# Optimization experiments

Hardware: AMD Instinct MI355X
Metric: run time of the kernel (lower is better)

## Reference

```python
import jax, jax.numpy as jnp
import numpy as np

B, N, DIM = 4, 2048, 512
H, DH = 8, 64  # n_heads, dim_head; inner = H*DH = 512
SCALE = DH ** -0.5


def setup_inputs() -> dict:
    key = jax.random.key(0)
    k1, k2, k3 = jax.random.split(key, 3)
    inner = H * DH
    X = jax.random.normal(k1, (B, N, DIM), dtype=jnp.float32)
    W_qkv = jax.random.normal(k2, (DIM, 3 * inner), dtype=jnp.float32) * (DIM ** -0.5)
    W_out = jax.random.normal(k3, (inner, DIM), dtype=jnp.float32) * (inner ** -0.5)
    b_out = jnp.zeros((DIM,), dtype=jnp.float32)
    return {"X": X, "W_qkv": W_qkv, "W_out": W_out, "b_out": b_out}


def reference(X, W_qkv, W_out, b_out):
    # X: (b, n, dim)
    qkv = X @ W_qkv                      # (b, n, 3*h*d)
    q, k, v = jnp.split(qkv, 3, axis=-1)
    def to_heads(t):
        b, n, _ = t.shape
        return t.reshape(b, n, H, DH).transpose(0, 2, 1, 3)  # (b, h, n, d)
    q, k, v = to_heads(q), to_heads(k), to_heads(v)
    # NOTE: original computes scores[n, m] = k_n . q_m and softmaxes over m (query axis)
    scores = jnp.einsum('bhnd,bhmd->bhnm', k, q) * SCALE     # (b, h, n_k, m_q)
    att = jax.nn.softmax(scores, axis=-1)
    # out token axis is the KEY index n: out[n, d] = sum_e att[n, e] * v[e, d]
    out = jnp.einsum('bhne,bhed->bhnd', att, v)              # (b, h, n, d)
    out = out.transpose(0, 2, 1, 3).reshape(X.shape[0], X.shape[1], H * DH)  # (b, n, h*d)
    return out @ W_out + b_out
```

## Files before the change

kernel.cpp:

```cpp
#include <hip/hip_runtime.h>
#include <hip/hip_bf16.h>

typedef __bf16 bf16_t;
typedef bf16_t bf16x8 __attribute__((ext_vector_type(8)));
typedef bf16_t bf16x4v __attribute__((ext_vector_type(4)));
typedef float f32x4 __attribute__((ext_vector_type(4)));
typedef float f32x16 __attribute__((ext_vector_type(16)));
typedef int i32x4 __attribute__((ext_vector_type(4)));

#define B_SZ 4
#define N_TOK 2048
#define DIM 512
#define H_N 8
#define DH 64
#define INNER 512
#define M_ROWS 8192
#define NQKV 1536
#define K_FOLD 0.18033688011112042f

#define GLD_LDS16(gp, lp)                                          \
  __builtin_amdgcn_global_load_lds(                                \
      (const __attribute__((address_space(1))) void*)(gp),         \
      (__attribute__((address_space(3))) void*)(lp), 16, 0, 0)

__device__ __forceinline__ float fexp2(float x) {
#if __has_builtin(__builtin_amdgcn_exp2f)
  return __builtin_amdgcn_exp2f(x);
#else
  float r;
  asm volatile("v_exp_f32 %0, %1\n\ts_nop 1" : "=v"(r) : "v"(x));
  return r;
#endif
}

__device__ __forceinline__ int cvtpk_bf16(float lo, float hi) {
  int r;
  asm("v_cvt_pk_bf16_f32 %0, %1, %2" : "=v"(r) : "v"(lo), "v"(hi));
  return r;
}

__device__ __forceinline__ void permswap32(int& a, int& b) {
  asm volatile("v_permlane32_swap_b32 %0, %1" : "+v"(a), "+v"(b));
}


__global__ void f32_to_bf16_kernel(const float* __restrict__ src,
                                   bf16_t* __restrict__ dst, int n4) {
  int i = blockIdx.x * blockDim.x + threadIdx.x;
  int stride = gridDim.x * blockDim.x;
  for (; i < n4; i += stride) {
    float4 f = reinterpret_cast<const float4*>(src)[i];
    bf16x4v o;
    o.x = (bf16_t)f.x; o.y = (bf16_t)f.y; o.z = (bf16_t)f.z; o.w = (bf16_t)f.w;
    reinterpret_cast<bf16x4v*>(dst)[i] = o;
  }
}

__global__ void transpose_f32_to_bf16_kernel(const float* __restrict__ src,
                                             bf16_t* __restrict__ dst, int R, int C) {
  int t = blockIdx.x * blockDim.x + threadIdx.x;
  if (t >= R * C) return;
  int r = t / C, c = t - r * C;
  dst[(size_t)c * R + r] = (bf16_t)src[t];
}

template <int MODE>
__global__ __launch_bounds__(256) void gemm_bf16_kernel(
    const bf16_t* __restrict__ A, const bf16_t* __restrict__ Bt,
    int M, int Nn, int K,
    bf16_t* __restrict__ qb, bf16_t* __restrict__ kb, bf16_t* __restrict__ vtb,
    float* __restrict__ outF, const float* __restrict__ bias) {
  __shared__ bf16_t As[128 * 64];
  __shared__ bf16_t Bs[128 * 64];

  const int tid = threadIdx.x;
  const int lane = tid & 63;
  const int wave = tid >> 6;
  const int g = lane >> 4, c = lane & 15;
  const int wm = (wave >> 1) * 64, wn = (wave & 1) * 64;
  const int m0 = blockIdx.x * 128, n0 = blockIdx.y * 128;

  f32x4 acc[4][4] = {};

  for (int k0 = 0; k0 < K; k0 += 64) {
    __syncthreads();
    #pragma unroll
    for (int i = 0; i < 4; ++i) {
      int blk = i * 256 + tid;
      int row = blk >> 3;
      int cb = (blk & 7) ^ (row & 7);
      int base = (i * 256 + wave * 64) * 8;
      GLD_LDS16(A + (size_t)(m0 + row) * K + k0 + cb * 8, &As[base]);
      GLD_LDS16(Bt + (size_t)(n0 + row) * K + k0 + cb * 8, &Bs[base]);
    }
    __syncthreads();
    __builtin_amdgcn_s_setprio(1);
    #pragma unroll
    for (int ks = 0; ks < 2; ++ks) {
      bf16x8 af[4], bfr[4];
      #pragma unroll
      for (int i = 0; i < 4; ++i) {
        af[i] = *reinterpret_cast<const bf16x8*>(
            &As[(wm + i * 16 + c) * 64 + (((ks * 4 + g) ^ (c & 7)) * 8)]);
        bfr[i] = *reinterpret_cast<const bf16x8*>(
            &Bs[(wn + i * 16 + c) * 64 + (((ks * 4 + g) ^ (c & 7)) * 8)]);
      }
      #pragma unroll
      for (int mi = 0; mi < 4; ++mi)
        #pragma unroll
        for (int ni = 0; ni < 4; ++ni)
          acc[mi][ni] = __builtin_amdgcn_mfma_f32_16x16x32_bf16(
              af[mi], bfr[ni], acc[mi][ni], 0, 0, 0);
    }
    __builtin_amdgcn_s_setprio(0);
  }

  #pragma unroll
  for (int mi = 0; mi < 4; ++mi) {
    #pragma unroll
    for (int ni = 0; ni < 4; ++ni) {
      int colg = n0 + wn + ni * 16 + c;
      if (MODE == 0) {
        int s = colg >> 9;
        int hh = (colg >> 6) & 7, dd = colg & 63;
        int rowg0 = m0 + wm + mi * 16 + g * 4;
        int bb = rowg0 >> 11, nn = rowg0 & 2047;
        if (s == 2) {
          bf16x4v pk;
          pk.x = (bf16_t)acc[mi][ni][0];
          pk.y = (bf16_t)acc[mi][ni][1];
          pk.z = (bf16_t)acc[mi][ni][2];
          pk.w = (bf16_t)acc[mi][ni][3];
          *reinterpret_cast<bf16x4v*>(
              &vtb[(((size_t)(bb * H_N + hh)) * DH + dd) * N_TOK + nn]) = pk;
        } else {
          float sc = (s == 1) ? K_FOLD : 1.0f;
          bf16_t* dst = (s == 0) ? qb : kb;
          #pragma unroll
          for (int r = 0; r < 4; ++r)
            dst[(((size_t)(bb * H_N + hh)) * N_TOK + nn + r) * DH + dd] =
                (bf16_t)(acc[mi][ni][r] * sc);
        }
      } else {
        #pragma unroll
        for (int r = 0; r < 4; ++r) {
          int rowg = m0 + wm + mi * 16 + g * 4 + r;
          outF[(size_t)rowg * Nn + colg] = acc[mi][ni][r] + bias[colg];
        }
      }
    }
  }
}

__global__ __launch_bounds__(256, 2) void attn_kernel(
    const bf16_t* __restrict__ Qproj, const bf16_t* __restrict__ Kproj,
    const bf16_t* __restrict__ Vt, bf16_t* __restrict__ att_out) {
  const int glin = blockIdx.x;
  const int xcd = glin & 7;
  const int jj = glin >> 3;
  const int hb = xcd * 4 + (jj >> 4);
  const int rb = jj & 15;
  const int h = hb & 7, b = hb >> 3;

  const size_t hbo = (size_t)(b * H_N + h);
  const bf16_t* Aq = Kproj + hbo * N_TOK * DH;
  const bf16_t* Ak = Qproj + hbo * N_TOK * DH;
  const bf16_t* Av = Vt + hbo * (size_t)DH * N_TOK;

  const int tid = threadIdx.x, lane = tid & 63, wave = tid >> 6;
  const int nl = lane & 31;
  const int hf = lane >> 5;
  const int r0 = rb * 128, wr0 = wave * 32;

  __shared__ bf16_t sK[2][64 * 64];
  __shared__ bf16_t sV[2][64 * 64];

  bf16x8 qreg[4];
  #pragma unroll
  for (int ks = 0; ks < 4; ++ks)
    qreg[ks] = *reinterpret_cast<const bf16x8*>(
        &Aq[(size_t)(r0 + wr0 + nl) * DH + ks * 16 + hf * 8]);

  f32x16 accO[2] = {};
  float Lp[2] = {0.f, 0.f};

  auto stage = [&](bf16_t* dK, bf16_t* dV, int j0) {
    #pragma unroll
    for (int i = 0; i < 2; ++i) {
      int blk = i * 256 + tid;
      int row = blk >> 3;
      int cb = (blk & 7) ^ (row & 7);
      int base = (i * 256 + wave * 64) * 8;
      GLD_LDS16(Ak + (size_t)(j0 + row) * DH + cb * 8, dK + base);
      GLD_LDS16(Av + (size_t)row * N_TOK + j0 + cb * 8, dV + base);
    }
  };

  stage(sK[0], sV[0], 0);
  __syncthreads();

  constexpr int NT = N_TOK / 64;
  for (int t = 0; t < NT; ++t) {
    if (t + 1 < NT) stage(sK[(t + 1) & 1], sV[(t + 1) & 1], (t + 1) * 64);
    const bf16_t* bK = sK[t & 1];
    const bf16_t* bV = sV[t & 1];

    f32x16 accT[2] = {};
    __builtin_amdgcn_s_setprio(1);
    #pragma unroll
    for (int ks = 0; ks < 4; ++ks) {
      bf16x8 ak0 = *reinterpret_cast<const bf16x8*>(
          &bK[nl * 64 + (((ks * 2 + hf) ^ (nl & 7)) * 8)]);
      bf16x8 ak1 = *reinterpret_cast<const bf16x8*>(
          &bK[(32 + nl) * 64 + (((ks * 2 + hf) ^ (nl & 7)) * 8)]);
      accT[0] = __builtin_amdgcn_mfma_f32_32x32x16_bf16(ak0, qreg[ks], accT[0], 0, 0, 0);
      accT[1] = __builtin_amdgcn_mfma_f32_32x32x16_bf16(ak1, qreg[ks], accT[1], 0, 0, 0);
    }
    __builtin_amdgcn_s_setprio(0);

    #pragma unroll
    for (int mi = 0; mi < 2; ++mi) {
      #pragma unroll
      for (int r = 0; r < 16; ++r) {
        float p = fexp2(accT[mi][r]);
        accT[mi][r] = p;
        Lp[mi] += p;
      }
    }

    __builtin_amdgcn_s_setprio(1);
    #pragma unroll
    for (int ks = 0; ks < 4; ++ks) {
      const int mi = ks >> 1, base = (ks & 1) * 8;
      int a0 = cvtpk_bf16(accT[mi][base + 0], accT[mi][base + 1]);
      int b0 = cvtpk_bf16(accT[mi][base + 4], accT[mi][base + 5]);
      int a1 = cvtpk_bf16(accT[mi][base + 2], accT[mi][base + 3]);
      int b1 = cvtpk_bf16(accT[mi][base + 6], accT[mi][base + 7]);
      permswap32(a0, b0);
      permswap32(a1, b1);
      i32x4 w; w.x = a0; w.y = a1; w.z = b0; w.w = b1;
      bf16x8 pfrag = __builtin_bit_cast(bf16x8, w);
      bf16x8 av0 = *reinterpret_cast<const bf16x8*>(
          &bV[nl * 64 + (((ks * 2 + hf) ^ (nl & 7)) * 8)]);
      bf16x8 av1 = *reinterpret_cast<const bf16x8*>(
          &bV[(32 + nl) * 64 + (((ks * 2 + hf) ^ (nl & 7)) * 8)]);
      accO[0] = __builtin_amdgcn_mfma_f32_32x32x16_bf16(av0, pfrag, accO[0], 0, 0, 0);
      accO[1] = __builtin_amdgcn_mfma_f32_32x32x16_bf16(av1, pfrag, accO[1], 0, 0, 0);
    }
    __builtin_amdgcn_s_setprio(0);

    __syncthreads();
  }

  float l = Lp[0] + Lp[1];
  l += __shfl_xor(l, 32);
  float invL = 1.0f / l;
  const int nrow = r0 + wr0 + nl;
  #pragma unroll
  for (int di = 0; di < 2; ++di) {
    #pragma unroll
    for (int q = 0; q < 4; ++q) {
      int d0 = 32 * di + 8 * q + 4 * hf;
      bf16x4v o;
      o.x = (bf16_t)(accO[di][4 * q + 0] * invL);
      o.y = (bf16_t)(accO[di][4 * q + 1] * invL);
      o.z = (bf16_t)(accO[di][4 * q + 2] * invL);
      o.w = (bf16_t)(accO[di][4 * q + 3] * invL);
      *reinterpret_cast<bf16x4v*>(
          &att_out[((size_t)(b * N_TOK) + nrow) * INNER + h * DH + d0]) = o;
    }
  }
}


extern "C" void kernel_launch(void* const* d_in, const int* in_sizes, int n_in,
                              void* d_out, int out_size, void* d_ws, size_t ws_size,
                              hipStream_t stream) {
  const float* X    = (const float*)d_in[0];
  const float* Wqkv = (const float*)d_in[1];
  const float* Wout = (const float*)d_in[2];
  const float* bout = (const float*)d_in[3];
  float* out = (float*)d_out;

  char* ws = (char*)d_ws;
  bf16_t* Xb    = (bf16_t*)(ws);
  bf16_t* WqkvT = (bf16_t*)(ws + 8388608);
  bf16_t* WoutT = (bf16_t*)(ws + 9961472);
  bf16_t* Qb    = (bf16_t*)(ws + 10485760);
  bf16_t* Kb    = (bf16_t*)(ws + 18874368);
  bf16_t* Vtb   = (bf16_t*)(ws + 27262976);
  bf16_t* AttO  = (bf16_t*)(ws + 35651584);

  f32_to_bf16_kernel<<<2048, 256, 0, stream>>>(X, Xb, (M_ROWS * DIM) / 4);
  transpose_f32_to_bf16_kernel<<<(DIM * NQKV + 255) / 256, 256, 0, stream>>>(
      Wqkv, WqkvT, DIM, NQKV);
  transpose_f32_to_bf16_kernel<<<(INNER * DIM + 255) / 256, 256, 0, stream>>>(
      Wout, WoutT, INNER, DIM);

  dim3 g1(M_ROWS / 128, NQKV / 128);
  gemm_bf16_kernel<0><<<g1, 256, 0, stream>>>(Xb, WqkvT, M_ROWS, NQKV, DIM,
                                              Qb, Kb, Vtb, nullptr, nullptr);

  attn_kernel<<<dim3(512), 256, 0, stream>>>(Qb, Kb, Vtb, AttO);

  dim3 g3(M_ROWS / 128, DIM / 128);
  gemm_bf16_kernel<1><<<g3, 256, 0, stream>>>(AttO, WoutT, M_ROWS, DIM, DIM,
                                              nullptr, nullptr, nullptr, out, bout);
}
```

Baseline: 95.02 us.

## Enlarge attention tiles to 256 rows per block and 128-key stages

Each wave now handles 64 output rows (two 32-row query sets) so every K/V fragment loaded from LDS feeds two MFMAs, and the key/value tile per stage grows from 64 to 128 with a new swizzle for the wider V tile. The grid halves to 256 blocks and launch bounds drop to one block per CU. The aim is to cut LDS traffic and barriers per unit of work. The cost is double the register and LDS footprint and only 256 blocks, which may underfill the 256 CUs and reduce latency hiding.

Result: slower. 98.34 us (+3.5%).

```diff
diff --git a/kernel.cpp b/kernel.cpp
--- a/kernel.cpp
+++ b/kernel.cpp
@@ -152,14 +152,14 @@
   }
 }
 
-__global__ __launch_bounds__(256, 2) void attn_kernel(
+__global__ __launch_bounds__(256, 1) void attn_kernel(
     const bf16_t* __restrict__ Qproj, const bf16_t* __restrict__ Kproj,
     const bf16_t* __restrict__ Vt, bf16_t* __restrict__ att_out) {
   const int glin = blockIdx.x;
   const int xcd = glin & 7;
   const int jj = glin >> 3;
-  const int hb = xcd * 4 + (jj >> 4);
-  const int rb = jj & 15;
+  const int hb = xcd * 4 + (jj >> 3);
+  const int rb = jj & 7;
   const int h = hb & 7, b = hb >> 3;
 
   const size_t hbo = (size_t)(b * H_N + h);
@@ -170,104 +170,129 @@
   const int tid = threadIdx.x, lane = tid & 63, wave = tid >> 6;
   const int nl = lane & 31;
   const int hf = lane >> 5;
-  const int r0 = rb * 128, wr0 = wave * 32;
-
-  __shared__ bf16_t sK[2][64 * 64];
-  __shared__ bf16_t sV[2][64 * 64];
-
-  bf16x8 qreg[4];
+  const int r0 = rb * 256, wr0 = wave * 64;
+
+  __shared__ bf16_t sK[2][128 * 64];
+  __shared__ bf16_t sV[2][64 * 128];
+
+  bf16x8 qreg[2][4];
   #pragma unroll
-  for (int ks = 0; ks < 4; ++ks)
-    qreg[ks] = *reinterpret_cast<const bf16x8*>(
-        &Aq[(size_t)(r0 + wr0 + nl) * DH + ks * 16 + hf * 8]);
-
-  f32x16 accO[2] = {};
-  float Lp[2] = {0.f, 0.f};
+  for (int cs = 0; cs < 2; ++cs)
+    #pragma unroll
+    for (int ks = 0; ks < 4; ++ks)
+      qreg[cs][ks] = *reinterpret_cast<const bf16x8*>(
+          &Aq[(size_t)(r0 + wr0 + cs * 32 + nl) * DH + ks * 16 + hf * 8]);
+
+  f32x16 accO[2][2] = {};
+  float Lp[2][2] = {};
 
   auto stage = [&](bf16_t* dK, bf16_t* dV, int j0) {
     #pragma unroll
-    for (int i = 0; i < 2; ++i) {
-      int blk = i * 256 + tid;
-      int row = blk >> 3;
-      int cb = (blk & 7) ^ (row & 7);
+    for (int i = 0; i < 4; ++i) {
+      int idx = i * 256 + tid;
       int base = (i * 256 + wave * 64) * 8;
-      GLD_LDS16(Ak + (size_t)(j0 + row) * DH + cb * 8, dK + base);
-      GLD_LDS16(Av + (size_t)row * N_TOK + j0 + cb * 8, dV + base);
+      int rowK = idx >> 3;
+      int cbK = (idx & 7) ^ (rowK & 7);
+      GLD_LDS16(Ak + (size_t)(j0 + rowK) * DH + cbK * 8, dK + base);
+      int rowV = idx >> 4;
+      int sv = idx & 15;
+      int pV = (sv & 8) | ((sv & 7) ^ (rowV & 7));
+      GLD_LDS16(Av + (size_t)rowV * N_TOK + j0 + pV * 8, dV + base);
     }
   };
 
   stage(sK[0], sV[0], 0);
   __syncthreads();
 
-  constexpr int NT = N_TOK / 64;
+  constexpr int NT = N_TOK / 128;
   for (int t = 0; t < NT; ++t) {
-    if (t + 1 < NT) stage(sK[(t + 1) & 1], sV[(t + 1) & 1], (t + 1) * 64);
+    if (t + 1 < NT) stage(sK[(t + 1) & 1], sV[(t + 1) & 1], (t + 1) * 128);
     const bf16_t* bK = sK[t & 1];
     const bf16_t* bV = sV[t & 1];
 
-    f32x16 accT[2] = {};
-    __builtin_amdgcn_s_setprio(1);
-    #pragma unroll
-    for (int ks = 0; ks < 4; ++ks) {
-      bf16x8 ak0 = *reinterpret_cast<const bf16x8*>(
-          &bK[nl * 64 + (((ks * 2 + hf) ^ (nl & 7)) * 8)]);
-      bf16x8 ak1 = *reinterpret_cast<const bf16x8*>(
-          &bK[(32 + nl) * 64 + (((ks * 2 + hf) ^ (nl & 7)) * 8)]);
-      accT[0] = __builtin_amdgcn_mfma_f32_32x32x16_bf16(ak0, qreg[ks], accT[0], 0, 0, 0);
-      accT[1] = __builtin_amdgcn_mfma_f32_32x32x16_bf16(ak1, qreg[ks], accT[1], 0, 0, 0);
-    }
-    __builtin_amdgcn_s_setprio(0);
-
-    #pragma unroll
-    for (int mi = 0; mi < 2; ++mi) {
-      #pragma unroll
-      for (int r = 0; r < 16; ++r) {
-        float p = fexp2(accT[mi][r]);
-        accT[mi][r] = p;
-        Lp[mi] += p;
-      }
-    }
-
-    __builtin_amdgcn_s_setprio(1);
-    #pragma unroll
-    for (int ks = 0; ks < 4; ++ks) {
-      const int mi = ks >> 1, base = (ks & 1) * 8;
-      int a0 = cvtpk_bf16(accT[mi][base + 0], accT[mi][base + 1]);
-      int b0 = cvtpk_bf16(accT[mi][base + 4], accT[mi][base + 5]);
-      int a1 = cvtpk_bf16(accT[mi][base + 2], accT[mi][base + 3]);
-      int b1 = cvtpk_bf16(accT[mi][base + 6], accT[mi][base + 7]);
-      permswap32(a0, b0);
-      permswap32(a1, b1);
-      i32x4 w; w.x = a0; w.y = a1; w.z = b0; w.w = b1;
-      bf16x8 pfrag = __builtin_bit_cast(bf16x8, w);
-      bf16x8 av0 = *reinterpret_cast<const bf16x8*>(
-          &bV[nl * 64 + (((ks * 2 + hf) ^ (nl & 7)) * 8)]);
-      bf16x8 av1 = *reinterpret_cast<const bf16x8*>(
-          &bV[(32 + nl) * 64 + (((ks * 2 + hf) ^ (nl & 7)) * 8)]);
-      accO[0] = __builtin_amdgcn_mfma_f32_32x32x16_bf16(av0, pfrag, accO[0], 0, 0, 0);
-      accO[1] = __builtin_amdgcn_mfma_f32_32x32x16_bf16(av1, pfrag, accO[1], 0, 0, 0);
-    }
-    __builtin_amdgcn_s_setprio(0);
+    #pragma unroll
+    for (int ch = 0; ch < 2; ++ch) {
+      f32x16 accT[2][2] = {};
+      __builtin_amdgcn_s_setprio(1);
+      #pragma unroll
+      for (int ks = 0; ks < 4; ++ks) {
+        #pragma unroll
+        for (int mi = 0; mi < 2; ++mi) {
+          int rowt = ch * 64 + mi * 32 + nl;
+          bf16x8 ak = *reinterpret_cast<const bf16x8*>(
+              &bK[rowt * 64 + (((ks * 2 + hf) ^ (rowt & 7)) * 8)]);
+          accT[0][mi] = __builtin_amdgcn_mfma_f32_32x32x16_bf16(
+              ak, qreg[0][ks], accT[0][mi], 0, 0, 0);
+          accT[1][mi] = __builtin_amdgcn_mfma_f32_32x32x16_bf16(
+              ak, qreg[1][ks], accT[1][mi], 0, 0, 0);
+        }
+      }
+      __builtin_amdgcn_s_setprio(0);
+
+      #pragma unroll
+      for (int cs = 0; cs < 2; ++cs)
+        #pragma unroll
+        for (int mi = 0; mi < 2; ++mi)
+          #pragma unroll
+          for (int r = 0; r < 16; ++r) {
+            float p = fexp2(accT[cs][mi][r]);
+            accT[cs][mi][r] = p;
+            Lp[cs][mi] += p;
+          }
+
+      __builtin_amdgcn_s_setprio(1);
+      #pragma unroll
+      for (int ks = 0; ks < 4; ++ks) {
+        bf16x8 av[2];
+        #pragma unroll
+        for (int vi = 0; vi < 2; ++vi) {
+          int rowv = vi * 32 + nl;
+          int pp = ch * 8 + ks * 2 + hf;
+          av[vi] = *reinterpret_cast<const bf16x8*>(
+              &bV[rowv * 128 + (((pp & 8) | ((pp & 7) ^ (rowv & 7))) * 8)]);
+        }
+        #pragma unroll
+        for (int cs = 0; cs < 2; ++cs) {
+          const int mi = ks >> 1, base = (ks & 1) * 8;
+          int a0 = cvtpk_bf16(accT[cs][mi][base + 0], accT[cs][mi][base + 1]);
+          int b0 = cvtpk_bf16(accT[cs][mi][base + 4], accT[cs][mi][base + 5]);
+          int a1 = cvtpk_bf16(accT[cs][mi][base + 2], accT[cs][mi][base + 3]);
+          int b1 = cvtpk_bf16(accT[cs][mi][base + 6], accT[cs][mi][base + 7]);
+          permswap32(a0, b0);
+          permswap32(a1, b1);
+          i32x4 w; w.x = a0; w.y = a1; w.z = b0; w.w = b1;
+          bf16x8 pfrag = __builtin_bit_cast(bf16x8, w);
+          accO[cs][0] = __builtin_amdgcn_mfma_f32_32x32x16_bf16(
+              av[0], pfrag, accO[cs][0], 0, 0, 0);
+          accO[cs][1] = __builtin_amdgcn_mfma_f32_32x32x16_bf16(
+              av[1], pfrag, accO[cs][1], 0, 0, 0);
+        }
+      }
+      __builtin_amdgcn_s_setprio(0);
+    }
 
     __syncthreads();
   }
 
-  float l = Lp[0] + Lp[1];
-  l += __shfl_xor(l, 32);
-  float invL = 1.0f / l;
-  const int nrow = r0 + wr0 + nl;
   #pragma unroll
-  for (int di = 0; di < 2; ++di) {
-    #pragma unroll
-    for (int q = 0; q < 4; ++q) {
-      int d0 = 32 * di + 8 * q + 4 * hf;
-      bf16x4v o;
-      o.x = (bf16_t)(accO[di][4 * q + 0] * invL);
-      o.y = (bf16_t)(accO[di][4 * q + 1] * invL);
-      o.z = (bf16_t)(accO[di][4 * q + 2] * invL);
-      o.w = (bf16_t)(accO[di][4 * q + 3] * invL);
-      *reinterpret_cast<bf16x4v*>(
-          &att_out[((size_t)(b * N_TOK) + nrow) * INNER + h * DH + d0]) = o;
+  for (int cs = 0; cs < 2; ++cs) {
+    float l = Lp[cs][0] + Lp[cs][1];
+    l += __shfl_xor(l, 32);
+    float invL = 1.0f / l;
+    const int nrow = r0 + wr0 + cs * 32 + nl;
+    #pragma unroll
+    for (int vi = 0; vi < 2; ++vi) {
+      #pragma unroll
+      for (int q = 0; q < 4; ++q) {
+        int d0 = 32 * vi + 8 * q + 4 * hf;
+        bf16x4v o;
+        o.x = (bf16_t)(accO[cs][vi][4 * q + 0] * invL);
+        o.y = (bf16_t)(accO[cs][vi][4 * q + 1] * invL);
+        o.z = (bf16_t)(accO[cs][vi][4 * q + 2] * invL);
+        o.w = (bf16_t)(accO[cs][vi][4 * q + 3] * invL);
+        *reinterpret_cast<bf16x4v*>(
+            &att_out[((size_t)(b * N_TOK) + nrow) * INNER + h * DH + d0]) = o;
+      }
     }
   }
 }
@@ -301,7 +326,7 @@
   gemm_bf16_kernel<0><<<g1, 256, 0, stream>>>(Xb, WqkvT, M_ROWS, NQKV, DIM,
                                               Qb, Kb, Vtb, nullptr, nullptr);
 
-  attn_kernel<<<dim3(512), 256, 0, stream>>>(Qb, Kb, Vtb, AttO);
+  attn_kernel<<<dim3(256), 256, 0, stream>>>(Qb, Kb, Vtb, AttO);
 
   dim3 g3(M_ROWS / 128, DIM / 128);
   gemm_bf16_kernel<1><<<g3, 256, 0, stream>>>(AttO, WoutT, M_ROWS, DIM, DIM,
```
